# Kernel tuning notes

Measured on AMD Instinct MI355X. Metric: run time of the kernel, lower is better.

## Reference

```python
import jax, jax.numpy as jnp
import numpy as np

B, C1, C2, NH, HC, EC, GC, NTXT, H, W = 8, 128, 128, 4, 32, 128, 512, 32, 160, 160
GA_HEADS, GA_HD, K_NN, NUM_SELECT = 4, 32, 6, 64  # graph attn: min(nh,4) heads, head_dim=C1/4
BN_EPS = 1e-5


def setup_inputs() -> dict:
    key = jax.random.key(0)
    ks = jax.random.split(key, 16)
    rn = lambda k, shape, s=0.05: jax.random.normal(k, shape, dtype=jnp.float32) * s
    return {
        'x': jax.random.normal(ks[0], (B, C1, H, W), dtype=jnp.float32),
        'guide': jax.random.normal(ks[1], (B, NTXT, GC), dtype=jnp.float32),
        'w_gm1': rn(ks[2], (C1 // 4, C1)), 'b_gm1': jnp.zeros((C1 // 4,), jnp.float32),
        'w_gm2': rn(ks[3], (GA_HEADS, C1 // 4)), 'b_gm2': jnp.zeros((GA_HEADS,), jnp.float32),
        'w_qkv': rn(ks[4], (3 * C1, C1)),
        'w_ge1': rn(ks[5], (C1 // 2, C1)), 'b_ge1': jnp.zeros((C1 // 2,), jnp.float32),
        'w_ge2': rn(ks[6], (GA_HEADS, C1 // 2)), 'b_ge2': jnp.zeros((GA_HEADS,), jnp.float32),
        'w_gl': rn(ks[7], (EC, GC)), 'b_gl': jnp.zeros((EC,), jnp.float32),
        'attn_bias': rn(ks[8], (NH,), 0.1),
        'w_proj': rn(ks[9], (C2, C1, 3, 3)),
        'bn_gamma': jnp.ones((C2,), jnp.float32), 'bn_beta': jnp.zeros((C2,), jnp.float32),
        'bn_mean': rn(ks[10], (C2,)),
        'bn_var': jax.random.uniform(ks[11], (C2,), jnp.float32, 0.5, 1.5),
    }


def _graph_attention(x, w_gm1, b_gm1, w_gm2, b_gm2, w_qkv, w_ge1, b_ge1, w_ge2, b_ge2):
    # EfficientGraphModulatedAttention.forward (eval mode, dropout off)
    b, c, h, w = x.shape
    # spatial modulation: 1x1 conv -> relu -> 1x1 conv -> sigmoid   [B,GA_HEADS,H,W]
    h1 = jax.nn.relu(jnp.einsum('bchw,oc->bohw', x, w_gm1) + b_gm1[None, :, None, None])
    sm = jax.nn.sigmoid(jnp.einsum('bchw,oc->bohw', h1, w_gm2) + b_gm2[None, :, None, None])
    # top-k important pixels per image (num_select = min(64, int(H*W*0.005)))
    imp = jnp.abs(x).mean(axis=1).reshape(b, h * w)
    _, top_idx = jax.lax.top_k(imp, NUM_SELECT)                       # [B,S]
    x_flat = x.reshape(b, c, h * w).transpose(0, 2, 1)                # [B,HW,C]
    sel = jnp.take_along_axis(x_flat, top_idx[:, :, None], axis=1)    # [B,S,C]

    def per_sample(feats):                                            # feats: [S,C]
        s = feats.shape[0]
        # KNN graph over cosine similarity; self-edges dropped (as in torch loop)
        nf = feats / jnp.clip(jnp.linalg.norm(feats, axis=1, keepdims=True), 1e-12)
        sim = nf @ nf.T                                               # [S,S]
        _, nbr = jax.lax.top_k(sim, K_NN + 1)                         # [S,K+1]
        src = jnp.repeat(jnp.arange(s), K_NN + 1)
        dst = nbr.reshape(-1)
        valid = src != dst
        # local multi-head attention over selected nodes
        qkv = (feats @ w_qkv.T).reshape(s, 3, GA_HEADS, GA_HD).transpose(1, 2, 0, 3)
        q, k, v = qkv[0], qkv[1], qkv[2]                              # [GA_HEADS,S,GA_HD]
        scores = jnp.einsum('hse,hte->hst', q, k) * (GA_HD ** -0.5)
        # edge modulation (identical for every head in the torch code)
        gw = jax.nn.relu(feats @ w_ge1.T + b_ge1) @ w_ge2.T + b_ge2   # [S,GA_HEADS]
        ew = (gw[src] * gw[dst]).mean(axis=-1)                        # [E]
        mod = jnp.zeros((s, s), feats.dtype).at[src, dst].set(jnp.where(valid, ew, 0.0))
        attn = jax.nn.softmax(scores + 0.1 * mod[None], axis=-1)
        return attn.mean(axis=(0, 2))                                 # pixel importance [S]

    pix = jax.vmap(per_sample)(sel)                                   # [B,S]
    gmw_flat = jnp.zeros((b, h * w), x.dtype).at[jnp.arange(b)[:, None], top_idx].set(pix)
    gmw = jnp.broadcast_to(gmw_flat.reshape(b, 1, h, w), (b, GA_HEADS, h, w))
    final_mod = 0.7 * sm + 0.3 * gmw
    return x * final_mod.mean(axis=1, keepdims=True)


def _forward(x, guide, w_gm1, b_gm1, w_gm2, b_gm2, w_qkv, w_ge1, b_ge1, w_ge2, b_ge2,
             w_gl, b_gl, attn_bias, w_proj, bn_gamma, bn_beta, bn_mean, bn_var):
    bs, _, h, w = x.shape
    x_mod = _graph_attention(x, w_gm1, b_gm1, w_gm2, b_gm2, w_qkv, w_ge1, b_ge1, w_ge2, b_ge2)
    x = x + 0.1 * x_mod
    g = (guide @ w_gl.T + b_gl).reshape(bs, -1, NH, HC)               # [B,n,NH,HC]
    embed = x.reshape(bs, NH, HC, h, w)                               # self.ec is None (c1==ec)
    aw = jnp.einsum('bmchw,bnmc->bmhwn', embed, g)
    aw = aw.max(axis=-1) / np.sqrt(HC).astype(np.float32)
    aw = jax.nn.sigmoid(aw + attn_bias[None, :, None, None]) * 1.0    # scale buffer == 1
    aw_single = aw.mean(axis=1)                                       # [B,H,W]
    xp = jax.lax.conv_general_dilated(x, w_proj, (1, 1), 'SAME',
                                      dimension_numbers=('NCHW', 'OIHW', 'NCHW'))
    s = bn_gamma / jnp.sqrt(bn_var + BN_EPS)                          # eval-mode BN
    xp = xp * s[None, :, None, None] + (bn_beta - bn_mean * s)[None, :, None, None]
    xp = xp.reshape(bs, NH, HC, h, w) * aw[:, :, None]
    return xp.reshape(bs, -1, h, w), aw_single


def reference(x, guide, w_gm1, b_gm1, w_gm2, b_gm2, w_qkv, w_ge1, b_ge1, w_ge2, b_ge2,
              w_gl, b_gl, attn_bias, w_proj, bn_gamma, bn_beta, bn_mean, bn_var):
    return _forward(x, guide, w_gm1, b_gm1, w_gm2, b_gm2, w_qkv, w_ge1, b_ge1, w_ge2, b_ge2,
                    w_gl, b_gl, attn_bias, w_proj, bn_gamma, bn_beta, bn_mean, bn_var)
```

## Files before the change

### kernel.cpp

```cpp
#include <hip/hip_runtime.h>
#include <hip/hip_bf16.h>
#include <math.h>

#define B_   8
#define C1_  128
#define H_   160
#define W_   160
#define HW_  25600
#define NSEL_ 64
#define BONUS_ 4.6875e-4f

typedef __attribute__((ext_vector_type(8))) unsigned short ushort8;
typedef __attribute__((ext_vector_type(8))) short short8;
typedef __attribute__((ext_vector_type(4))) float f32x4;

#define OFF_FAC 0
#define OFF_IMP 819200
#define OFF_AW4 1638400
#define OFF_G   4915200
#define OFF_TB  5046272
#define OFF_WT  5046784
#define OFF_WPK 5636608
#define OFF_XH  5931520
#define WS_NEED_FAST 58360320ULL

__device__ __forceinline__ float sigmoidf_(float v) {
    return 1.0f / (1.0f + expf(-v));
}
__device__ __forceinline__ unsigned short f2bf(float f) {
    unsigned u = __float_as_uint(f);
    return (unsigned short)((u + 0x7fffu + ((u >> 16) & 1u)) >> 16);
}
__device__ __forceinline__ float bf2f(unsigned short h) {
    return __uint_as_float(((unsigned)h) << 16);
}

__global__ void k0_wt(const float* __restrict__ wp, const float* __restrict__ gamma,
                      const float* __restrict__ beta, const float* __restrict__ mean,
                      const float* __restrict__ var, float* __restrict__ wt,
                      float* __restrict__ tb) {
    int i = blockIdx.x * 256 + threadIdx.x;
    if (i < 128) {
        float s = gamma[i] * rsqrtf(var[i] + 1e-5f);
        tb[i] = beta[i] - mean[i] * s;
    }
    if (i < 128 * 128 * 9) {
        int o  = i & 127;
        int it = i >> 7;
        float s = gamma[o] * rsqrtf(var[o] + 1e-5f);
        wt[i] = wp[o * 1152 + it] * s;
    }
}

__global__ void k0b_pack(const float* __restrict__ wp, const float* __restrict__ gamma,
                         const float* __restrict__ var, unsigned short* __restrict__ wpk) {
    int idx = blockIdx.x * 256 + threadIdx.x;
    if (idx >= 147456) return;
    int j = idx & 7, l = (idx >> 3) & 63, f = idx >> 9;
    int kstep = f >> 3, mblk = f & 7;
    int tap = kstep >> 2, icb = kstep & 3;
    int oc = mblk * 16 + (l & 15);
    int ic = icb * 32 + ((l >> 4) << 3) + j;
    float s = gamma[oc] * rsqrtf(var[oc] + 1e-5f);
    wpk[idx] = f2bf(wp[oc * 1152 + ic * 9 + tap] * s);
}

__global__ __launch_bounds__(256) void k1a_convert(const float* __restrict__ x,
                                                   float* __restrict__ imp,
                                                   unsigned short* __restrict__ xh) {
    __shared__ float red[4][256];
    const int tid = threadIdx.x;
    const int l = tid & 63, g = tid >> 6;
    const int px0 = blockIdx.x * 256;
    const int b = blockIdx.y;
    const int pxl = l * 4;
    const float* xb = x + (size_t)b * C1_ * HW_ + px0 + pxl;
    unsigned short* xrb = xh + ((size_t)(b * HW_ + px0 + pxl)) * 128 + g * 32;

    float sab0 = 0.f, sab1 = 0.f, sab2 = 0.f, sab3 = 0.f;
    ushort8 v0, v1, v2, v3;
#pragma unroll
    for (int j = 0; j < 32; ++j) {
        float4 xv = *reinterpret_cast<const float4*>(xb + (size_t)(g * 32 + j) * HW_);
        sab0 += fabsf(xv.x); sab1 += fabsf(xv.y);
        sab2 += fabsf(xv.z); sab3 += fabsf(xv.w);
        const int jj = j & 7;
        v0[jj] = f2bf(xv.x); v1[jj] = f2bf(xv.y);
        v2[jj] = f2bf(xv.z); v3[jj] = f2bf(xv.w);
        if (jj == 7) {
            const int gr = j & ~7;
            *reinterpret_cast<ushort8*>(xrb + 0 * 128 + gr) = v0;
            *reinterpret_cast<ushort8*>(xrb + 1 * 128 + gr) = v1;
            *reinterpret_cast<ushort8*>(xrb + 2 * 128 + gr) = v2;
            *reinterpret_cast<ushort8*>(xrb + 3 * 128 + gr) = v3;
        }
    }
    red[g][pxl + 0] = sab0; red[g][pxl + 1] = sab1;
    red[g][pxl + 2] = sab2; red[g][pxl + 3] = sab3;
    __syncthreads();
    imp[b * HW_ + px0 + tid] =
        (red[0][tid] + red[1][tid] + red[2][tid] + red[3][tid]) * (1.f / 128.f);
}

__global__ __launch_bounds__(256) void k1_mod(const float* __restrict__ x,
                                              const float* __restrict__ w_gm1,
                                              const float* __restrict__ b_gm1,
                                              const float* __restrict__ w_gm2,
                                              const float* __restrict__ b_gm2,
                                              float* __restrict__ fac,
                                              float* __restrict__ imp,
                                              unsigned short* __restrict__ xh,
                                              int wxh) {
    __shared__ float4 w1t[128 * 8];
    __shared__ float  b1s[32];
    __shared__ float  w2s[128];
    __shared__ float  b2s[4];
    const int tid = threadIdx.x;
    for (int i = tid; i < 4096; i += 256) {
        int j = i >> 7, c = i & 127;
        ((float*)w1t)[c * 32 + j] = w_gm1[i];
    }
    if (tid < 32) b1s[tid] = b_gm1[tid];
    if (tid < 128) w2s[tid] = w_gm2[tid];
    if (tid < 4) b2s[tid] = b_gm2[tid];
    __syncthreads();

    const int hw0 = blockIdx.x * 512 + tid * 2;
    const int b = blockIdx.y;
    const float* xb = x + (size_t)b * C1_ * HW_ + hw0;
    unsigned short* xrow = xh + ((size_t)b * HW_ + hw0) * 128;

    float h[2][32];
#pragma unroll
    for (int j = 0; j < 32; ++j) { h[0][j] = 0.f; h[1][j] = 0.f; }
    float sab0 = 0.f, sab1 = 0.f;
    for (int c8 = 0; c8 < 16; ++c8) {
        ushort8 v0, v1;
#pragma unroll
        for (int k = 0; k < 8; ++k) {
            int c = c8 * 8 + k;
            float2 xv = *reinterpret_cast<const float2*>(xb + (size_t)c * HW_);
            sab0 += fabsf(xv.x);
            sab1 += fabsf(xv.y);
            v0[k] = f2bf(xv.x);
            v1[k] = f2bf(xv.y);
            const float4* wr = &w1t[c * 8];
#pragma unroll
            for (int j4 = 0; j4 < 8; ++j4) {
                float4 w = wr[j4];
                h[0][j4 * 4 + 0] += xv.x * w.x; h[0][j4 * 4 + 1] += xv.x * w.y;
                h[0][j4 * 4 + 2] += xv.x * w.z; h[0][j4 * 4 + 3] += xv.x * w.w;
                h[1][j4 * 4 + 0] += xv.y * w.x; h[1][j4 * 4 + 1] += xv.y * w.y;
                h[1][j4 * 4 + 2] += xv.y * w.z; h[1][j4 * 4 + 3] += xv.y * w.w;
            }
        }
        if (wxh) {
            *reinterpret_cast<ushort8*>(xrow + c8 * 8) = v0;
            *reinterpret_cast<ushort8*>(xrow + 128 + c8 * 8) = v1;
        }
    }
#pragma unroll
    for (int p = 0; p < 2; ++p) {
        float fm = 0.f;
#pragma unroll
        for (int j = 0; j < 32; ++j) h[p][j] = fmaxf(h[p][j] + b1s[j], 0.f);
#pragma unroll
        for (int m = 0; m < 4; ++m) {
            float s = b2s[m];
#pragma unroll
            for (int j = 0; j < 32; ++j) s += w2s[m * 32 + j] * h[p][j];
            fm += sigmoidf_(s);
        }
        fac[b * HW_ + hw0 + p] = 1.f + 0.07f * (fm * 0.25f);
        imp[b * HW_ + hw0 + p] = (p == 0 ? sab0 : sab1) * (1.f / 128.f);
    }
}

__device__ __forceinline__ int blockReduceSum1024(int v, int* red, int tid) {
#pragma unroll
    for (int off = 32; off >= 1; off >>= 1) v += __shfl_down(v, off);
    if ((tid & 63) == 0) red[tid >> 6] = v;
    __syncthreads();
    if (tid < 64) {
        int s = (tid < 16) ? red[tid] : 0;
#pragma unroll
        for (int off = 8; off >= 1; off >>= 1) s += __shfl_down(s, off);
        if (tid == 0) red[16] = s;
    }
    __syncthreads();
    int r = red[16];
    __syncthreads();
    return r;
}

__global__ __launch_bounds__(1024) void k2_topk(const float* __restrict__ imp,
                                                float* __restrict__ fac) {
    __shared__ int red[17];
    __shared__ int claimed;
    const int tid = threadIdx.x;
    const int b = blockIdx.x;
    unsigned u[25];
#pragma unroll
    for (int i = 0; i < 25; ++i)
        u[i] = __float_as_uint(imp[b * HW_ + i * 1024 + tid]);

    unsigned cur = 0u;
    for (int bit = 30; bit >= 0; --bit) {
        unsigned cand = cur | (1u << bit);
        int c = 0;
#pragma unroll
        for (int i = 0; i < 25; ++i) c += (u[i] >= cand) ? 1 : 0;
        int tot = blockReduceSum1024(c, red, tid);
        if (tot >= NSEL_) cur = cand;
    }
    int cg = 0;
#pragma unroll
    for (int i = 0; i < 25; ++i) cg += (u[i] > cur) ? 1 : 0;
    int tot_gt = blockReduceSum1024(cg, red, tid);
    int need = NSEL_ - tot_gt;
    if (tid == 0) claimed = 0;
    __syncthreads();
#pragma unroll
    for (int i = 0; i < 25; ++i) {
        int idx = i * 1024 + tid;
        if (u[i] > cur) {
            fac[b * HW_ + idx] += BONUS_;
        } else if (u[i] == cur) {
            int c = atomicAdd(&claimed, 1);
            if (c < need) fac[b * HW_ + idx] += BONUS_;
        }
    }
}

__global__ __launch_bounds__(128) void k3_guide(const float* __restrict__ guide,
                                                const float* __restrict__ w_gl,
                                                const float* __restrict__ b_gl,
                                                float* __restrict__ g) {
    __shared__ float gr[512];
    const int bn = blockIdx.x;
    const int tid = threadIdx.x;
    for (int i = tid; i < 512; i += 128) gr[i] = guide[bn * 512 + i];
    __syncthreads();
    const float4* w4 = (const float4*)(w_gl + (size_t)tid * 512);
    const float4* g4 = (const float4*)gr;
    float acc = b_gl[tid];
    for (int k = 0; k < 128; ++k) {
        float4 w = w4[k]; float4 v = g4[k];
        acc += w.x * v.x + w.y * v.y + w.z * v.z + w.w * v.w;
    }
    g[bn * 128 + tid] = acc;
}

__global__ __launch_bounds__(256) void k4m2_scores(const unsigned short* __restrict__ xh,
                                                   const float* __restrict__ g,
                                                   const float* __restrict__ w_gm1,
                                                   const float* __restrict__ b_gm1,
                                                   const float* __restrict__ w_gm2,
                                                   const float* __restrict__ b_gm2,
                                                   float* __restrict__ mx4,
                                                   float* __restrict__ fac) {
    __shared__ unsigned short xs[128 * 128];
    const int tid = threadIdx.x;
    const int l = tid & 63, w = tid >> 6;
    const int px0 = blockIdx.x * 128;
    const int b = blockIdx.y;

#pragma unroll
    for (int i = 0; i < 8; ++i) {
        int idx = i * 256 + tid;
        int row = idx >> 4, gg = idx & 15;
        const char* src = (const char*)(xh + ((size_t)(b * HW_ + px0 + row)) * 128
                                        + ((gg ^ (row & 7)) * 8));
        char* dst = (char*)xs + (size_t)(i * 4096 + w * 1024);
        __builtin_amdgcn_global_load_lds((const unsigned int*)src,
                                         (unsigned int*)dst, 16, 0, 0);
    }

    const int lr = l & 15, lk = l >> 4;

    short8 afr[4][2];
#pragma unroll
    for (int m = 0; m < 4; ++m)
#pragma unroll
        for (int nb = 0; nb < 2; ++nb) {
            const float* gp = g + (size_t)b * 4096 + (nb * 16 + lr) * 128
                              + m * 32 + (lk << 3);
            float4 g0 = *reinterpret_cast<const float4*>(gp);
            float4 g1 = *reinterpret_cast<const float4*>(gp + 4);
            short8 a;
            a[0] = (short)f2bf(g0.x); a[1] = (short)f2bf(g0.y);
            a[2] = (short)f2bf(g0.z); a[3] = (short)f2bf(g0.w);
            a[4] = (short)f2bf(g1.x); a[5] = (short)f2bf(g1.y);
            a[6] = (short)f2bf(g1.z); a[7] = (short)f2bf(g1.w);
            afr[m][nb] = a;
        }

    short8 w1f[2][4];
#pragma unroll
    for (int ob = 0; ob < 2; ++ob)
#pragma unroll
        for (int kb = 0; kb < 4; ++kb) {
            const float* wp = w_gm1 + (size_t)(ob * 16 + lr) * 128 + kb * 32 + (lk << 3);
            float4 g0 = *reinterpret_cast<const float4*>(wp);
            float4 g1 = *reinterpret_cast<const float4*>(wp + 4);
            short8 a;
            a[0] = (short)f2bf(g0.x); a[1] = (short)f2bf(g0.y);
            a[2] = (short)f2bf(g0.z); a[3] = (short)f2bf(g0.w);
            a[4] = (short)f2bf(g1.x); a[5] = (short)f2bf(g1.y);
            a[6] = (short)f2bf(g1.z); a[7] = (short)f2bf(g1.w);
            w1f[ob][kb] = a;
        }

    float b1r[8], w2r[4][8];
#pragma unroll
    for (int r = 0; r < 4; ++r) {
        b1r[r] = b_gm1[lk * 4 + r];
        b1r[4 + r] = b_gm1[16 + lk * 4 + r];
    }
#pragma unroll
    for (int m = 0; m < 4; ++m)
#pragma unroll
        for (int r = 0; r < 4; ++r) {
            w2r[m][r] = w_gm2[m * 32 + lk * 4 + r];
            w2r[m][4 + r] = w_gm2[m * 32 + 16 + lk * 4 + r];
        }
    const float b20 = b_gm2[0], b21 = b_gm2[1], b22 = b_gm2[2], b23 = b_gm2[3];

    __syncthreads();

#pragma unroll
    for (int pxb = 0; pxb < 2; ++pxb) {
        const int px = (w * 2 + pxb) * 16 + lr;
        float mr[4];
        f32x4 h0{0.f, 0.f, 0.f, 0.f}, h1{0.f, 0.f, 0.f, 0.f};
#pragma unroll
        for (int m = 0; m < 4; ++m) {
            int gl = (m * 4 + lk) ^ (px & 7);
            short8 bf = *reinterpret_cast<const short8*>(xs + (size_t)px * 128 + gl * 8);
            f32x4 a0{0.f, 0.f, 0.f, 0.f}, a1{0.f, 0.f, 0.f, 0.f};
            a0 = __builtin_amdgcn_mfma_f32_16x16x32_bf16(afr[m][0], bf, a0, 0, 0, 0);
            a1 = __builtin_amdgcn_mfma_f32_16x16x32_bf16(afr[m][1], bf, a1, 0, 0, 0);
            h0 = __builtin_amdgcn_mfma_f32_16x16x32_bf16(w1f[0][m], bf, h0, 0, 0, 0);
            h1 = __builtin_amdgcn_mfma_f32_16x16x32_bf16(w1f[1][m], bf, h1, 0, 0, 0);
            float v = fmaxf(fmaxf(fmaxf(a0[0], a0[1]), fmaxf(a0[2], a0[3])),
                            fmaxf(fmaxf(a1[0], a1[1]), fmaxf(a1[2], a1[3])));
            v = fmaxf(v, __shfl_xor(v, 16));
            v = fmaxf(v, __shfl_xor(v, 32));
            mr[m] = v;
        }
        float s0 = b20, s1 = b21, s2 = b22, s3 = b23;
#pragma unroll
        for (int r = 0; r < 4; ++r) {
            float hv0 = fmaxf(h0[r] + b1r[r], 0.f);
            float hv1 = fmaxf(h1[r] + b1r[4 + r], 0.f);
            s0 += w2r[0][r] * hv0 + w2r[0][4 + r] * hv1;
            s1 += w2r[1][r] * hv0 + w2r[1][4 + r] * hv1;
            s2 += w2r[2][r] * hv0 + w2r[2][4 + r] * hv1;
            s3 += w2r[3][r] * hv0 + w2r[3][4 + r] * hv1;
        }
        s0 += __shfl_xor(s0, 16); s0 += __shfl_xor(s0, 32);
        s1 += __shfl_xor(s1, 16); s1 += __shfl_xor(s1, 32);
        s2 += __shfl_xor(s2, 16); s2 += __shfl_xor(s2, 32);
        s3 += __shfl_xor(s3, 16); s3 += __shfl_xor(s3, 32);
        float fm = sigmoidf_(s0) + sigmoidf_(s1) + sigmoidf_(s2) + sigmoidf_(s3);
        if (l < 16) {
            float4 o; o.x = mr[0]; o.y = mr[1]; o.z = mr[2]; o.w = mr[3];
            int hw = px0 + (w * 2 + pxb) * 16 + l;
            *reinterpret_cast<float4*>(mx4 + (size_t)(b * HW_ + hw) * 4) = o;
            fac[b * HW_ + hw] = 1.f + 0.0175f * fm;
        }
    }
}

__global__ __launch_bounds__(256) void k4c_aw(const float* __restrict__ mx4,
                                              const float* __restrict__ fac,
                                              const float* __restrict__ attn_bias,
                                              float* __restrict__ aw4,
                                              float* __restrict__ aw_single) {
    const int hw = blockIdx.x * 256 + threadIdx.x;
    const int b = blockIdx.y;
    float4 mv = *reinterpret_cast<const float4*>(mx4 + (size_t)(b * HW_ + hw) * 4);
    float facv = fac[b * HW_ + hw] * 0.17677669529663687f;
    float b0 = attn_bias[0], b1 = attn_bias[1], b2 = attn_bias[2], b3 = attn_bias[3];
    float a0 = sigmoidf_(mv.x * facv + b0);
    float a1 = sigmoidf_(mv.y * facv + b1);
    float a2 = sigmoidf_(mv.z * facv + b2);
    float a3 = sigmoidf_(mv.w * facv + b3);
    aw4[((size_t)(b * 4 + 0)) * HW_ + hw] = a0;
    aw4[((size_t)(b * 4 + 1)) * HW_ + hw] = a1;
    aw4[((size_t)(b * 4 + 2)) * HW_ + hw] = a2;
    aw4[((size_t)(b * 4 + 3)) * HW_ + hw] = a3;
    aw_single[b * HW_ + hw] = (a0 + a1 + a2 + a3) * 0.25f;
}

__global__ __launch_bounds__(256) void k4_aw(const float* __restrict__ x,
                                             const float* __restrict__ fac,
                                             const float* __restrict__ g,
                                             const float* __restrict__ attn_bias,
                                             float* __restrict__ aw4,
                                             float* __restrict__ aw_single) {
    __shared__ float gl[4096];
    __shared__ float biass[4];
    const int tid = threadIdx.x;
    const int b = blockIdx.y;
    for (int i = tid; i < 4096; i += 256) {
        int n = i >> 7, e = i & 127;
        gl[e * 32 + n] = g[b * 4096 + i];
    }
    if (tid < 4) biass[tid] = attn_bias[tid];
    __syncthreads();
    const int hw = blockIdx.x * 256 + tid;
    const float facv = fac[b * HW_ + hw];
    const float* xb = x + (size_t)b * C1_ * HW_ + hw;
    float asum = 0.f;
#pragma unroll
    for (int m = 0; m < 4; ++m) {
        float acc[32];
#pragma unroll
        for (int n = 0; n < 32; ++n) acc[n] = 0.f;
        for (int c = 0; c < 32; ++c) {
            float xv = xb[(m * 32 + c) * HW_] * facv;
            const float4* grow = (const float4*)&gl[(m * 32 + c) * 32];
#pragma unroll
            for (int n4 = 0; n4 < 8; ++n4) {
                float4 gv = grow[n4];
                acc[n4 * 4 + 0] += xv * gv.x; acc[n4 * 4 + 1] += xv * gv.y;
                acc[n4 * 4 + 2] += xv * gv.z; acc[n4 * 4 + 3] += xv * gv.w;
            }
        }
        float mxv = acc[0];
#pragma unroll
        for (int n = 1; n < 32; ++n) mxv = fmaxf(mxv, acc[n]);
        float awv = sigmoidf_(mxv * 0.17677669529663687f + biass[m]);
        aw4[((size_t)(b * 4 + m)) * HW_ + hw] = awv;
        asum += awv;
    }
    aw_single[b * HW_ + hw] = asum * 0.25f;
}

__global__ __launch_bounds__(256) void k5_mfma(const unsigned short* __restrict__ xh,
                                               const float* __restrict__ fac,
                                               const unsigned short* __restrict__ wpk,
                                               const float* __restrict__ tb,
                                               const float* __restrict__ aw4,
                                               float* __restrict__ out) {
    __shared__ unsigned short xs[180 * 17 * 8];
    const int tid = threadIdx.x;
    const int l = tid & 63, w = tid >> 6;
    const int bx0 = blockIdx.x * 16;
    const int by0 = blockIdx.y * 8;
    const int b   = blockIdx.z;

    for (int i = tid; i < 2880; i += 256) {
        int gg = i & 15, pc = i >> 4;
        int hc = pc % 18, hr = pc / 18;
        int gy = by0 - 1 + hr, gx = bx0 - 1 + hc;
        ushort8 v;
#pragma unroll
        for (int k = 0; k < 8; ++k) v[k] = 0;
        if (gy >= 0 && gy < H_ && gx >= 0 && gx < W_) {
            int hw = gy * W_ + gx;
            v = *reinterpret_cast<const ushort8*>(xh + ((size_t)b * HW_ + hw) * 128 + gg * 8);
            float fv = fac[b * HW_ + hw];
#pragma unroll
            for (int k = 0; k < 8; ++k) v[k] = f2bf(bf2f(v[k]) * fv);
        }
        *reinterpret_cast<ushort8*>(xs + (size_t)(pc * 17 + gg) * 8) = v;
    }
    __syncthreads();

    const int mhalf = w >> 1, nhalf = w & 1;
    const int lr = l & 15, lk = l >> 4;

    f32x4 acc[4][4];
#pragma unroll
    for (int mf = 0; mf < 4; ++mf)
#pragma unroll
        for (int nf = 0; nf < 4; ++nf)
#pragma unroll
            for (int r = 0; r < 4; ++r) acc[mf][nf][r] = 0.f;

    const unsigned short* wlane = wpk + (size_t)(mhalf * 4) * 512 + (size_t)l * 8;
    short8 aC[4], aN[4];
#pragma unroll
    for (int mf = 0; mf < 4; ++mf)
        aC[mf] = *reinterpret_cast<const short8*>(wlane + mf * 512);

    for (int kstep = 0; kstep < 36; ++kstep) {
        if (kstep < 35) {
            const unsigned short* wk = wlane + (size_t)(kstep + 1) * 4096;
#pragma unroll
            for (int mf = 0; mf < 4; ++mf)
                aN[mf] = *reinterpret_cast<const short8*>(wk + mf * 512);
        }
        const int tap = kstep >> 2, icb = kstep & 3;
        const int dy = (tap >= 6) ? 2 : (tap >= 3 ? 1 : 0);
        const int dx = tap - dy * 3;
        const int hcl = lr + dx;
        short8 bf[4];
#pragma unroll
        for (int nf = 0; nf < 4; ++nf) {
            int hr = nhalf * 4 + nf + dy;
            bf[nf] = *reinterpret_cast<const short8*>(
                xs + (size_t)((hr * 18 + hcl) * 17 + icb * 4 + lk) * 8);
        }
#pragma unroll
        for (int mf = 0; mf < 4; ++mf)
#pragma unroll
            for (int nf = 0; nf < 4; ++nf)
                acc[mf][nf] = __builtin_amdgcn_mfma_f32_16x16x32_bf16(
                    aC[mf], bf[nf], acc[mf][nf], 0, 0, 0);
        if (kstep < 35) {
#pragma unroll
            for (int mf = 0; mf < 4; ++mf) aC[mf] = aN[mf];
        }
    }

    const float* awb = aw4 + (size_t)b * 4 * HW_;
    float* outb = out + (size_t)b * 128 * HW_;
#pragma unroll
    for (int mf = 0; mf < 4; ++mf) {
        const int ocb = mhalf * 64 + mf * 16;
        const int oc0 = ocb + lk * 4;
        const int head = ocb >> 5;
#pragma unroll
        for (int nf = 0; nf < 4; ++nf) {
            int px = nhalf * 64 + nf * 16 + lr;
            int hw = (by0 + (px >> 4)) * W_ + bx0 + (px & 15);
            float aw = awb[(size_t)head * HW_ + hw];
#pragma unroll
            for (int r = 0; r < 4; ++r) {
                int oc = oc0 + r;
                outb[(size_t)oc * HW_ + hw] = (acc[mf][nf][r] + tb[oc]) * aw;
            }
        }
    }
}

__global__ __launch_bounds__(256) void k5_conv(const float* __restrict__ x,
                                               const float* __restrict__ fac,
                                               const float* __restrict__ wt,
                                               const float* __restrict__ tb,
                                               const float* __restrict__ aw4,
                                               float* __restrict__ out) {
    __shared__ float ft[18][36];
    __shared__ float xs[16][18][36];
    __shared__ float wl[16][9][32];
    const int tx = threadIdx.x;
    const int ty = threadIdx.y;
    const int tid = ty * 32 + tx;
    const int bx0 = blockIdx.x * 32;
    const int by0 = blockIdx.y * 16;
    const int m = blockIdx.z & 3;
    const int b = blockIdx.z >> 2;

    for (int i = tid; i < 18 * 34; i += 256) {
        int r = i / 34, c = i - r * 34;
        int gy = by0 - 1 + r, gx = bx0 - 1 + c;
        bool in = (gy >= 0) && (gy < H_) && (gx >= 0) && (gx < W_);
        ft[r][c] = in ? fac[b * HW_ + gy * W_ + gx] : 0.f;
    }
    float acc0[32], acc1[32];
#pragma unroll
    for (int i = 0; i < 32; ++i) { acc0[i] = 0.f; acc1[i] = 0.f; }
    __syncthreads();

    for (int icc = 0; icc < 8; ++icc) {
        const int ic0 = icc * 16;
        for (int i = tid; i < 4608; i += 256) {
            int ic = i / 288; int rem = i - ic * 288;
            int tap = rem >> 5; int oc = rem & 31;
            wl[ic][tap][oc] = wt[((ic0 + ic) * 9 + tap) * 128 + m * 32 + oc];
        }
        for (int i = tid; i < 16 * 612; i += 256) {
            int ic = i / 612; int j = i - ic * 612;
            int r = j / 34; int c = j - r * 34;
            int gy = by0 - 1 + r, gx = bx0 - 1 + c;
            int gyc = min(max(gy, 0), H_ - 1), gxc = min(max(gx, 0), W_ - 1);
            xs[ic][r][c] = x[((size_t)(b * C1_ + ic0 + ic)) * HW_ + gyc * W_ + gxc] * ft[r][c];
        }
        __syncthreads();
        for (int ic = 0; ic < 16; ++ic) {
#pragma unroll
            for (int ky = 0; ky < 3; ++ky) {
#pragma unroll
                for (int kx = 0; kx < 3; ++kx) {
                    float xv0 = xs[ic][ty + ky][tx + kx];
                    float xv1 = xs[ic][ty + 8 + ky][tx + kx];
                    const float4* wp = (const float4*)&wl[ic][ky * 3 + kx][0];
#pragma unroll
                    for (int o4 = 0; o4 < 8; ++o4) {
                        float4 wv = wp[o4];
                        acc0[o4 * 4 + 0] += xv0 * wv.x; acc0[o4 * 4 + 1] += xv0 * wv.y;
                        acc0[o4 * 4 + 2] += xv0 * wv.z; acc0[o4 * 4 + 3] += xv0 * wv.w;
                        acc1[o4 * 4 + 0] += xv1 * wv.x; acc1[o4 * 4 + 1] += xv1 * wv.y;
                        acc1[o4 * 4 + 2] += xv1 * wv.z; acc1[o4 * 4 + 3] += xv1 * wv.w;
                    }
                }
            }
        }
        __syncthreads();
    }

    const int hw0 = (by0 + ty) * W_ + bx0 + tx;
    const int hw1 = (by0 + ty + 8) * W_ + bx0 + tx;
    const float aw0 = aw4[((size_t)(b * 4 + m)) * HW_ + hw0];
    const float aw1 = aw4[((size_t)(b * 4 + m)) * HW_ + hw1];
    float* ob = out + ((size_t)(b * C1_ + m * 32)) * HW_;
#pragma unroll
    for (int oc = 0; oc < 32; ++oc) {
        float t = tb[m * 32 + oc];
        ob[oc * HW_ + hw0] = (acc0[oc] + t) * aw0;
        ob[oc * HW_ + hw1] = (acc1[oc] + t) * aw1;
    }
}

extern "C" void kernel_launch(void* const* d_in, const int* in_sizes, int n_in,
                              void* d_out, int out_size, void* d_ws, size_t ws_size,
                              hipStream_t stream) {
    const float* x        = (const float*)d_in[0];
    const float* guide    = (const float*)d_in[1];
    const float* w_gm1    = (const float*)d_in[2];
    const float* b_gm1    = (const float*)d_in[3];
    const float* w_gm2    = (const float*)d_in[4];
    const float* b_gm2    = (const float*)d_in[5];
    const float* w_gl     = (const float*)d_in[11];
    const float* b_gl     = (const float*)d_in[12];
    const float* attn_bias= (const float*)d_in[13];
    const float* w_proj   = (const float*)d_in[14];
    const float* bn_gamma = (const float*)d_in[15];
    const float* bn_beta  = (const float*)d_in[16];
    const float* bn_mean  = (const float*)d_in[17];
    const float* bn_var   = (const float*)d_in[18];

    char* wsb = (char*)d_ws;
    float* fac = (float*)(wsb + OFF_FAC);
    float* imp = (float*)(wsb + OFF_IMP);
    float* aw4 = (float*)(wsb + OFF_AW4);
    float* g   = (float*)(wsb + OFF_G);
    float* tb  = (float*)(wsb + OFF_TB);
    float* wt  = (float*)(wsb + OFF_WT);
    unsigned short* wpk = (unsigned short*)(wsb + OFF_WPK);
    unsigned short* xh  = (unsigned short*)(wsb + OFF_XH);

    float* out0 = (float*)d_out;
    float* out1 = (float*)d_out + (size_t)B_ * C1_ * HW_;
    float* mx4  = (float*)d_out;

    const bool fast = (ws_size >= WS_NEED_FAST);

    k0_wt<<<dim3(576), dim3(256), 0, stream>>>(w_proj, bn_gamma, bn_beta, bn_mean, bn_var, wt, tb);
    if (fast) {
        k0b_pack<<<dim3(576), dim3(256), 0, stream>>>(w_proj, bn_gamma, bn_var, wpk);
        k1a_convert<<<dim3(100, 8), dim3(256), 0, stream>>>(x, imp, xh);
        k3_guide<<<dim3(256), dim3(128), 0, stream>>>(guide, w_gl, b_gl, g);
        k4m2_scores<<<dim3(200, 8), dim3(256), 0, stream>>>(xh, g, w_gm1, b_gm1,
                                                            w_gm2, b_gm2, mx4, fac);
        k2_topk<<<dim3(8), dim3(1024), 0, stream>>>(imp, fac);
        k4c_aw<<<dim3(100, 8), dim3(256), 0, stream>>>(mx4, fac, attn_bias, aw4, out1);
        k5_mfma<<<dim3(10, 20, 8), dim3(256), 0, stream>>>(xh, fac, wpk, tb, aw4, out0);
    } else {
        k1_mod<<<dim3(50, 8), dim3(256), 0, stream>>>(x, w_gm1, b_gm1, w_gm2, b_gm2,
                                                      fac, imp, xh, 0);
        k3_guide<<<dim3(256), dim3(128), 0, stream>>>(guide, w_gl, b_gl, g);
        k2_topk<<<dim3(8), dim3(1024), 0, stream>>>(imp, fac);
        k4_aw<<<dim3(100, 8), dim3(256), 0, stream>>>(x, fac, g, attn_bias, aw4, out1);
        k5_conv<<<dim3(5, 10, B_ * 4), dim3(32, 8), 0, stream>>>(x, fac, wt, tb, aw4, out0);
    }
}
```

Measured before the change: 227.2 us.

## Pre-scale bf16 activations by modulation factor in score kernel, drop scaling from conv halo load

The score kernel now writes the modulation-scaled bf16 activations back into xh from its shared tile, and the top-k kernel rescales the few selected pixel rows by the bonus ratio. The MFMA conv kernel then loads xh directly without reading fac or doing per-element multiply and re-rounding in its halo staging loop, which it repeated for overlapping tiles. In exchange, the score kernel performs an extra full write pass of xh, and double bf16 rounding on the selected pixels slightly changes numerics.

After: 285.7 us. 1.26x slower.

```diff
diff --git a/kernel.cpp b/kernel.cpp
--- a/kernel.cpp
+++ b/kernel.cpp
@@ -108,9 +108,7 @@
                                               const float* __restrict__ w_gm2,
                                               const float* __restrict__ b_gm2,
                                               float* __restrict__ fac,
-                                              float* __restrict__ imp,
-                                              unsigned short* __restrict__ xh,
-                                              int wxh) {
+                                              float* __restrict__ imp) {
     __shared__ float4 w1t[128 * 8];
     __shared__ float  b1s[32];
     __shared__ float  w2s[128];
@@ -128,22 +126,18 @@
     const int hw0 = blockIdx.x * 512 + tid * 2;
     const int b = blockIdx.y;
     const float* xb = x + (size_t)b * C1_ * HW_ + hw0;
-    unsigned short* xrow = xh + ((size_t)b * HW_ + hw0) * 128;
 
     float h[2][32];
 #pragma unroll
     for (int j = 0; j < 32; ++j) { h[0][j] = 0.f; h[1][j] = 0.f; }
     float sab0 = 0.f, sab1 = 0.f;
     for (int c8 = 0; c8 < 16; ++c8) {
-        ushort8 v0, v1;
 #pragma unroll
         for (int k = 0; k < 8; ++k) {
             int c = c8 * 8 + k;
             float2 xv = *reinterpret_cast<const float2*>(xb + (size_t)c * HW_);
             sab0 += fabsf(xv.x);
             sab1 += fabsf(xv.y);
-            v0[k] = f2bf(xv.x);
-            v1[k] = f2bf(xv.y);
             const float4* wr = &w1t[c * 8];
 #pragma unroll
             for (int j4 = 0; j4 < 8; ++j4) {
@@ -154,10 +148,6 @@
                 h[1][j4 * 4 + 2] += xv.y * w.z; h[1][j4 * 4 + 3] += xv.y * w.w;
             }
         }
-        if (wxh) {
-            *reinterpret_cast<ushort8*>(xrow + c8 * 8) = v0;
-            *reinterpret_cast<ushort8*>(xrow + 128 + c8 * 8) = v1;
-        }
     }
 #pragma unroll
     for (int p = 0; p < 2; ++p) {
@@ -193,8 +183,28 @@
     return r;
 }
 
+__device__ __forceinline__ void bump_px(float* __restrict__ fac,
+                                        unsigned short* __restrict__ xh,
+                                        int b, int idx, int rescale) {
+    float fo = fac[b * HW_ + idx];
+    fac[b * HW_ + idx] = fo + BONUS_;
+    if (rescale) {
+        float ratio = (fo + BONUS_) / fo;
+        ushort8* row = reinterpret_cast<ushort8*>(xh + ((size_t)(b * HW_ + idx)) * 128);
+#pragma unroll
+        for (int g = 0; g < 16; ++g) {
+            ushort8 v = row[g];
+#pragma unroll
+            for (int k = 0; k < 8; ++k) v[k] = f2bf(bf2f(v[k]) * ratio);
+            row[g] = v;
+        }
+    }
+}
+
 __global__ __launch_bounds__(1024) void k2_topk(const float* __restrict__ imp,
-                                                float* __restrict__ fac) {
+                                                float* __restrict__ fac,
+                                                unsigned short* __restrict__ xh,
+                                                int rescale) {
     __shared__ int red[17];
     __shared__ int claimed;
     const int tid = threadIdx.x;
@@ -224,10 +234,10 @@
     for (int i = 0; i < 25; ++i) {
         int idx = i * 1024 + tid;
         if (u[i] > cur) {
-            fac[b * HW_ + idx] += BONUS_;
+            bump_px(fac, xh, b, idx, rescale);
         } else if (u[i] == cur) {
             int c = atomicAdd(&claimed, 1);
-            if (c < need) fac[b * HW_ + idx] += BONUS_;
+            if (c < need) bump_px(fac, xh, b, idx, rescale);
         }
     }
 }
@@ -251,7 +261,7 @@
     g[bn * 128 + tid] = acc;
 }
 
-__global__ __launch_bounds__(256) void k4m2_scores(const unsigned short* __restrict__ xh,
+__global__ __launch_bounds__(256) void k4m2_scores(unsigned short* __restrict__ xh,
                                                    const float* __restrict__ g,
                                                    const float* __restrict__ w_gm1,
                                                    const float* __restrict__ b_gm1,
@@ -260,6 +270,7 @@
                                                    float* __restrict__ mx4,
                                                    float* __restrict__ fac) {
     __shared__ unsigned short xs[128 * 128];
+    __shared__ float facs[128];
     const int tid = threadIdx.x;
     const int l = tid & 63, w = tid >> 6;
     const int px0 = blockIdx.x * 128;
@@ -366,8 +377,26 @@
         if (l < 16) {
             float4 o; o.x = mr[0]; o.y = mr[1]; o.z = mr[2]; o.w = mr[3];
             int hw = px0 + (w * 2 + pxb) * 16 + l;
+            float fv = 1.f + 0.0175f * fm;
             *reinterpret_cast<float4*>(mx4 + (size_t)(b * HW_ + hw) * 4) = o;
-            fac[b * HW_ + hw] = 1.f + 0.0175f * fm;
+            fac[b * HW_ + hw] = fv;
+            facs[(w * 2 + pxb) * 16 + l] = fv;
+        }
+    }
+
+    __syncthreads();
+    {
+        const int px = tid >> 1, hf = tid & 1;
+        const float fv = facs[px];
+        unsigned short* dst = xh + ((size_t)(b * HW_ + px0 + px)) * 128 + hf * 64;
+#pragma unroll
+        for (int gq = 0; gq < 8; ++gq) {
+            int G = hf * 8 + gq;
+            int slot = G ^ (px & 7);
+            ushort8 v = *reinterpret_cast<const ushort8*>(xs + (size_t)(px * 16 + slot) * 8);
+#pragma unroll
+            for (int k = 0; k < 8; ++k) v[k] = f2bf(bf2f(v[k]) * fv);
+            *reinterpret_cast<ushort8*>(dst + gq * 8) = v;
         }
     }
 }
@@ -439,7 +468,6 @@
 }
 
 __global__ __launch_bounds__(256) void k5_mfma(const unsigned short* __restrict__ xh,
-                                               const float* __restrict__ fac,
                                                const unsigned short* __restrict__ wpk,
                                                const float* __restrict__ tb,
                                                const float* __restrict__ aw4,
@@ -458,13 +486,9 @@
         ushort8 v;
 #pragma unroll
         for (int k = 0; k < 8; ++k) v[k] = 0;
-        if (gy >= 0 && gy < H_ && gx >= 0 && gx < W_) {
-            int hw = gy * W_ + gx;
-            v = *reinterpret_cast<const ushort8*>(xh + ((size_t)b * HW_ + hw) * 128 + gg * 8);
-            float fv = fac[b * HW_ + hw];
-#pragma unroll
-            for (int k = 0; k < 8; ++k) v[k] = f2bf(bf2f(v[k]) * fv);
-        }
+        if (gy >= 0 && gy < H_ && gx >= 0 && gx < W_)
+            v = *reinterpret_cast<const ushort8*>(
+                xh + ((size_t)(b * HW_ + gy * W_ + gx)) * 128 + gg * 8);
         *reinterpret_cast<ushort8*>(xs + (size_t)(pc * 17 + gg) * 8) = v;
     }
     __syncthreads();
@@ -656,14 +680,14 @@
         k3_guide<<<dim3(256), dim3(128), 0, stream>>>(guide, w_gl, b_gl, g);
         k4m2_scores<<<dim3(200, 8), dim3(256), 0, stream>>>(xh, g, w_gm1, b_gm1,
                                                             w_gm2, b_gm2, mx4, fac);
-        k2_topk<<<dim3(8), dim3(1024), 0, stream>>>(imp, fac);
+        k2_topk<<<dim3(8), dim3(1024), 0, stream>>>(imp, fac, xh, 1);
         k4c_aw<<<dim3(100, 8), dim3(256), 0, stream>>>(mx4, fac, attn_bias, aw4, out1);
-        k5_mfma<<<dim3(10, 20, 8), dim3(256), 0, stream>>>(xh, fac, wpk, tb, aw4, out0);
+        k5_mfma<<<dim3(10, 20, 8), dim3(256), 0, stream>>>(xh, wpk, tb, aw4, out0);
     } else {
         k1_mod<<<dim3(50, 8), dim3(256), 0, stream>>>(x, w_gm1, b_gm1, w_gm2, b_gm2,
-                                                      fac, imp, xh, 0);
+                                                      fac, imp);
         k3_guide<<<dim3(256), dim3(128), 0, stream>>>(guide, w_gl, b_gl, g);
-        k2_topk<<<dim3(8), dim3(1024), 0, stream>>>(imp, fac);
+        k2_topk<<<dim3(8), dim3(1024), 0, stream>>>(imp, fac, nullptr, 0);
         k4_aw<<<dim3(100, 8), dim3(256), 0, stream>>>(x, fac, g, attn_bias, aw4, out1);
         k5_conv<<<dim3(5, 10, B_ * 4), dim3(32, 8), 0, stream>>>(x, fac, wt, tb, aw4, out0);
     }
```
